# Optimization experiments

Hardware: AMD Instinct MI355X
Metric: run time of the kernel (lower is better)

The kernel has to match this reference:

```python
import jax, jax.numpy as jnp
import numpy as np

B = 8
H1c = W1c = 56
H2c = W2c = 112
C1 = 512
C2 = 256
NH = 8
WS = 7
POOL = 2
EPS = 1e-5


def setup_inputs() -> dict:
    key = jax.random.key(0)
    ks = jax.random.split(key, 8)
    x = jax.random.normal(ks[0], (B, H1c * W1c, C1), dtype=jnp.float32)
    y = jax.random.normal(ks[1], (B, H2c * W2c, C2), dtype=jnp.float32)
    Wq = jax.random.normal(ks[2], (C1, C1), dtype=jnp.float32) * 0.02
    Wkv = jax.random.normal(ks[3], (2 * C1, C2), dtype=jnp.float32) * 0.02
    Wproj = jax.random.normal(ks[4], (C1, C1), dtype=jnp.float32) * 0.02
    bproj = jnp.zeros((C1,), dtype=jnp.float32)
    # 1x1 conv: fan_out = out_channels -> std = sqrt(2/C2)
    Wsr = jax.random.normal(ks[5], (C2, C2), dtype=jnp.float32) * np.sqrt(2.0 / C2).astype(np.float32)
    bsr = jnp.zeros((C2,), dtype=jnp.float32)
    gn = jnp.ones((C2,), dtype=jnp.float32)
    bn = jnp.zeros((C2,), dtype=jnp.float32)
    return {"x": x, "y": y, "Wq": Wq, "Wkv": Wkv, "Wproj": Wproj,
            "bproj": bproj, "Wsr": Wsr, "bsr": bsr, "gn": gn, "bn": bn,
            "H1": H1c, "W1": W1c, "H2": H2c, "W2": W2c}


def _window_partition(t, ws):
    # t: (B, nh, H, W, C) -> (B*nh, num_windows, ws*ws, C)
    Bt, n, H, W, C = t.shape
    ht, wt = H // ws, W // ws
    t = t.reshape(Bt, n, ht, ws, wt, ws, C).transpose(0, 1, 2, 4, 3, 5, 6)
    return t.reshape(Bt * n, ht * wt, ws * ws, C)


def reference(x, y, Wq, Wkv, Wproj, bproj, Wsr, bsr, gn, bn, H1, W1, H2, W2):
    B1, N1, c1 = x.shape
    B2, N2, c2 = y.shape
    nh, ws = NH, WS
    hd = c1 // nh
    scale = hd ** (-0.5)

    # q projection -> (B, nh, H1, W1, hd)
    q = (x @ Wq.T).reshape(B1, H1, W1, nh, hd).transpose(0, 3, 1, 2, 4)

    # KV preprocessing: avgpool -> 1x1 conv -> layernorm -> gelu
    y2 = y.transpose(0, 2, 1).reshape(B2, c2, H2, W2)
    Hp, Wp = H2 // POOL, W2 // POOL
    y2 = y2.reshape(B2, c2, Hp, POOL, Wp, POOL).mean(axis=(3, 5))
    y2 = jnp.einsum('bchw,oc->bohw', y2, Wsr) + bsr[None, :, None, None]
    y2 = y2.reshape(B2, c2, Hp * Wp).transpose(0, 2, 1)  # (B, Np, C2)
    mu = y2.mean(-1, keepdims=True)
    var = y2.var(-1, keepdims=True)
    y2 = (y2 - mu) / jnp.sqrt(var + EPS) * gn + bn
    y2 = jax.nn.gelu(y2, approximate=False)

    kv = (y2 @ Wkv.T).reshape(B2, Hp * Wp, 2, nh, hd)
    k = kv[:, :, 0].transpose(0, 2, 1, 3).reshape(B2, nh, Hp, Wp, hd)
    v = kv[:, :, 1].transpose(0, 2, 1, 3).reshape(B2, nh, Hp, Wp, hd)

    qw = _window_partition(q, ws)   # (B*nh, nw, ws^2, hd)
    kw = _window_partition(k, ws)
    vw = _window_partition(v, ws)

    attn = jax.nn.softmax(jnp.einsum('bnqd,bnkd->bnqk', qw, kw) * scale, axis=-1)
    out = jnp.einsum('bnqk,bnkd->bnqd', attn, vw)  # (B*nh, nw, ws^2, hd)

    # window reverse -> (B, N1, C1)
    ht, wt = H1 // ws, W1 // ws
    out = out.reshape(B1, nh, ht, wt, ws, ws, hd).transpose(0, 1, 2, 4, 3, 5, 6)
    out = out.reshape(B1, nh, H1 * W1, hd).transpose(0, 2, 1, 3).reshape(B1, H1 * W1, c1)
    return out @ Wproj.T + bproj
```

## Files before the change

### kernel.cpp

```cpp
#include <hip/hip_runtime.h>
#include <hip/hip_bf16.h>

typedef __attribute__((ext_vector_type(8))) short short8;
typedef __attribute__((ext_vector_type(4))) float f32x4;
typedef __attribute__((ext_vector_type(4))) unsigned short ushort4v;

#define DI __device__ __forceinline__

DI unsigned short f2bf(float f) {
  union { float f; unsigned int u; } a; a.f = f;
  unsigned int u = a.u;
  return (unsigned short)((u + 0x7FFFu + ((u >> 16) & 1u)) >> 16);
}

#define BARRIER() do { asm volatile("" ::: "memory"); __builtin_amdgcn_s_barrier(); asm volatile("" ::: "memory"); } while (0)
#define GLOAD16(src, dst) __builtin_amdgcn_global_load_lds( \
    (const __attribute__((address_space(1))) void*)(src), \
    (__attribute__((address_space(3))) void*)(dst), 16, 0, 0)


__global__ __launch_bounds__(256)
void cvt_pool(const float* __restrict__ y, unsigned short* __restrict__ pooled,
              const float* __restrict__ Wq, const float* __restrict__ Wkv,
              const float* __restrict__ Wproj, const float* __restrict__ Wsr,
              unsigned short* __restrict__ Wq_b, unsigned short* __restrict__ Wkv_b,
              unsigned short* __restrict__ Wproj_b, unsigned short* __restrict__ Wsr_b) {
  int bid = blockIdx.x;
  if (bid < 6272) {
    int t = bid * 256 + threadIdx.x;
    int cv = (t & 63) * 4;
    int bp = t >> 6;
    int b = bp / 3136, p = bp % 3136;
    int hp = p / 56, wp = p % 56;
    const float* src = y + (((size_t)b * 12544) + hp * 224 + wp * 2) * 256 + cv;
    float4 a0 = *(const float4*)(src);
    float4 a1 = *(const float4*)(src + 256);
    float4 a2 = *(const float4*)(src + 28672);
    float4 a3 = *(const float4*)(src + 28672 + 256);
    float4 av;
    av.x = (a0.x + a1.x + a2.x + a3.x) * 0.25f;
    av.y = (a0.y + a1.y + a2.y + a3.y) * 0.25f;
    av.z = (a0.z + a1.z + a2.z + a3.z) * 0.25f;
    av.w = (a0.w + a1.w + a2.w + a3.w) * 0.25f;
    ushort4v o = { f2bf(av.x), f2bf(av.y), f2bf(av.z), f2bf(av.w) };
    *(ushort4v*)&pooled[(size_t)bp * 256 + cv] = o;
  } else {
    long i = (long)(bid - 6272) * 1024 + threadIdx.x * 4;
    const float* src; unsigned short* dst; long off;
    if (i < 262144L)      { src = Wq;    dst = Wq_b;    off = i; }
    else if (i < 524288L) { src = Wkv;   dst = Wkv_b;   off = i - 262144L; }
    else if (i < 786432L) { src = Wproj; dst = Wproj_b; off = i - 524288L; }
    else                  { src = Wsr;   dst = Wsr_b;   off = i - 786432L; }
    float4 v = *(const float4*)&src[off];
    ushort4v o = { f2bf(v.x), f2bf(v.y), f2bf(v.z), f2bf(v.w) };
    *(ushort4v*)&dst[off] = o;
  }
}

__global__ __launch_bounds__(256)
void sr_gemm(const unsigned short* __restrict__ Ap, const unsigned short* __restrict__ Wsr_b,
             const float* __restrict__ bsr, const float* __restrict__ gn,
             const float* __restrict__ bn, unsigned short* __restrict__ out) {
  __shared__ unsigned short sA[64 * 64];
  __shared__ unsigned short sB[256 * 64];
  __shared__ float red[64 * 8];

  const int tid = threadIdx.x;
  const int wv = tid >> 6;
  const int lane = tid & 63;
  const int lr = lane & 15;
  const int lg = lane >> 4;
  const int lr4 = lg * 4;
  const int m0 = blockIdx.x * 64;
  const int sr8 = lane >> 3;
  const int sl8 = lane & 7;

  f32x4 acc[4][4];
#pragma unroll
  for (int i = 0; i < 4; ++i)
#pragma unroll
    for (int j = 0; j < 4; ++j) acc[i][j] = (f32x4){0.f, 0.f, 0.f, 0.f};

  for (int kt = 0; kt < 256; kt += 64) {
#pragma unroll
    for (int c = 0; c < 2; ++c) {
      int row = wv * 16 + c * 8 + sr8;
      GLOAD16(Ap + (size_t)(m0 + row) * 256 + kt + ((sl8 ^ (row & 7)) * 8),
              &sA[(wv * 16 + c * 8) * 64]);
    }
#pragma unroll
    for (int c = 0; c < 8; ++c) {
      int row = wv * 64 + c * 8 + sr8;
      GLOAD16(Wsr_b + (size_t)row * 256 + kt + ((sl8 ^ (row & 7)) * 8),
              &sB[(wv * 64 + c * 8) * 64]);
    }
    __syncthreads();
#pragma unroll
    for (int ks = 0; ks < 2; ++ks) {
      short8 af[4], bfr[4];
#pragma unroll
      for (int i = 0; i < 4; ++i)
        af[i] = *(const short8*)&sA[(i * 16 + lr) * 64 + (((ks * 4 + lg) ^ (lr & 7)) * 8)];
#pragma unroll
      for (int j = 0; j < 4; ++j)
        bfr[j] = *(const short8*)&sB[(wv * 64 + j * 16 + lr) * 64 + (((ks * 4 + lg) ^ (lr & 7)) * 8)];
#pragma unroll
      for (int i = 0; i < 4; ++i)
#pragma unroll
        for (int j = 0; j < 4; ++j)
          acc[i][j] = __builtin_amdgcn_mfma_f32_16x16x32_bf16(af[i], bfr[j], acc[i][j], 0, 0, 0);
    }
    __syncthreads();
  }

  float bsv[4], gnv[4], bnv[4];
#pragma unroll
  for (int j = 0; j < 4; ++j) {
    int col = wv * 64 + j * 16 + lr;
    bsv[j] = bsr[col]; gnv[j] = gn[col]; bnv[j] = bn[col];
  }
  float s_[4][4], q_[4][4];
#pragma unroll
  for (int i = 0; i < 4; ++i)
#pragma unroll
    for (int r = 0; r < 4; ++r) {
      float s = 0.f, q = 0.f;
#pragma unroll
      for (int j = 0; j < 4; ++j) {
        float v = acc[i][j][r] + bsv[j];
        acc[i][j][r] = v;
        s += v; q += v * v;
      }
      s_[i][r] = s; q_[i][r] = q;
    }
#pragma unroll
  for (int m = 1; m <= 8; m <<= 1)
#pragma unroll
    for (int i = 0; i < 4; ++i)
#pragma unroll
      for (int r = 0; r < 4; ++r) {
        s_[i][r] += __shfl_xor(s_[i][r], m);
        q_[i][r] += __shfl_xor(q_[i][r], m);
      }
  if (lr == 0) {
#pragma unroll
    for (int i = 0; i < 4; ++i)
#pragma unroll
      for (int r = 0; r < 4; ++r) {
        int row = i * 16 + lr4 + r;
        red[row * 8 + wv * 2 + 0] = s_[i][r];
        red[row * 8 + wv * 2 + 1] = q_[i][r];
      }
  }
  __syncthreads();
#pragma unroll
  for (int i = 0; i < 4; ++i) {
#pragma unroll
    for (int r = 0; r < 4; ++r) {
      int row = i * 16 + lr4 + r;
      float sum = red[row * 8 + 0] + red[row * 8 + 2] + red[row * 8 + 4] + red[row * 8 + 6];
      float sq  = red[row * 8 + 1] + red[row * 8 + 3] + red[row * 8 + 5] + red[row * 8 + 7];
      float mean = sum * (1.f / 256.f);
      float var = sq * (1.f / 256.f) - mean * mean;
      float rstd = rsqrtf(var + 1e-5f);
#pragma unroll
      for (int j = 0; j < 4; ++j) {
        float t = (acc[i][j][r] - mean) * rstd * gnv[j] + bnv[j];
        t = 0.5f * t * (1.f + erff(t * 0.70710678118654752f));
        out[(size_t)(m0 + row) * 256 + wv * 64 + j * 16 + lr] = f2bf(t);
      }
    }
  }
}

DI void epi_q(int gm, int gc, float v, unsigned short* outp) {
  const int b = gm / 3136, pos = gm % 3136;
  const int h = pos / 56, ww = pos % 56;
  const int head = gc >> 6, d = gc & 63;
  const size_t idx = ((((size_t)(b * 8 + head)) * 64 + (h / 7) * 8 + (ww / 7)) * 49
                      + (h % 7) * 7 + (ww % 7)) * 64 + d;
  outp[idx] = f2bf(v);
}

template<int K, int N>
__global__ __launch_bounds__(512, 2)
void gemm256f(const float* __restrict__ A,
              const unsigned short* __restrict__ Bw,
              unsigned short* __restrict__ outp) {
  __shared__ unsigned short lds[65536];
  const int tid = threadIdx.x;
  const int wv = tid >> 6;
  const int lane = tid & 63;
  const int wm = wv >> 2;
  const int wn = wv & 3;
  const int m0 = blockIdx.y * 256;
  const int n0 = blockIdx.x * 256;
  const int lr = lane & 15;
  const int lg = lane >> 4;
  const int lr4 = lg * 4;
  const int srow8 = lane >> 3;
  const int sl8 = lane & 7;
  constexpr int NT = K / 64;

  f32x4 acc[8][4];
#pragma unroll
  for (int i = 0; i < 8; ++i)
#pragma unroll
    for (int j = 0; j < 4; ++j) acc[i][j] = (f32x4){0.f, 0.f, 0.f, 0.f};

  float4 fa[4][2];
  auto loadA = [&](int t1) {
    int tsrc = (t1 < NT) ? t1 : NT - 1;
#pragma unroll
    for (int rr = 0; rr < 4; ++rr) {
      int trow = rr * 64 + wv * 8 + srow8;
      const float* p = A + (size_t)(m0 + trow) * K + tsrc * 64 + sl8 * 8;
      fa[rr][0] = *(const float4*)p;
      fa[rr][1] = *(const float4*)(p + 4);
    }
    asm volatile("" ::: "memory");
  };
  auto writeA = [&](int t1) {
#pragma unroll
    for (int rr = 0; rr < 4; ++rr) {
      int trow = rr * 64 + wv * 8 + srow8;
      union { short8 s; unsigned short u[8]; } w;
      w.u[0] = f2bf(fa[rr][0].x); w.u[1] = f2bf(fa[rr][0].y);
      w.u[2] = f2bf(fa[rr][0].z); w.u[3] = f2bf(fa[rr][0].w);
      w.u[4] = f2bf(fa[rr][1].x); w.u[5] = f2bf(fa[rr][1].y);
      w.u[6] = f2bf(fa[rr][1].z); w.u[7] = f2bf(fa[rr][1].w);
      *(short8*)&lds[(t1 & 1) * 32768 + trow * 64 + ((sl8 ^ (trow & 7)) * 8)] = w.s;
    }
  };
  auto stageB = [&](int t1, int rr) {
    int tsrc = (t1 < NT) ? t1 : NT - 1;
    int trow = rr * 64 + wv * 8 + srow8;
    int sx = sl8 ^ (trow & 7);
    GLOAD16(Bw + (size_t)(n0 + trow) * K + tsrc * 64 + sx * 8,
            &lds[(t1 & 1) * 32768 + 16384 + (rr * 64 + wv * 8) * 64]);
  };
  auto rdA = [&](int s, int mf, int ks) -> short8 {
    int row = wm * 128 + mf * 16 + lr;
    int slot = ((ks << 2) + lg) ^ (row & 7);
    return *(const short8*)&lds[s * 32768 + row * 64 + slot * 8];
  };
  auto rdB = [&](int s, int nf, int ks) -> short8 {
    int row = wn * 64 + nf * 16 + lr;
    int slot = ((ks << 2) + lg) ^ (row & 7);
    return *(const short8*)&lds[s * 32768 + 16384 + row * 64 + slot * 8];
  };

  stageB(0, 0); stageB(0, 1); stageB(0, 2); stageB(0, 3);
  loadA(0);
  asm volatile("s_waitcnt vmcnt(0)" ::: "memory");
  writeA(0);
  asm volatile("s_waitcnt lgkmcnt(0)" ::: "memory");
  BARRIER();

  for (int t = 0; t < NT; ++t) {
    const int s = t & 1;
    short8 bfr[4][2];
    loadA(t + 1);
#pragma unroll
    for (int j = 0; j < 4; ++j) { bfr[j][0] = rdB(s, j, 0); bfr[j][1] = rdB(s, j, 1); }
    {
      short8 x0 = rdA(s, 0, 0), x1 = rdA(s, 0, 1);
      short8 y0 = rdA(s, 1, 0), y1 = rdA(s, 1, 1);
      BARRIER();
      __builtin_amdgcn_s_setprio(1);
#pragma unroll
      for (int j = 0; j < 4; ++j) {
        acc[0][j] = __builtin_amdgcn_mfma_f32_16x16x32_bf16(x0, bfr[j][0], acc[0][j], 0, 0, 0);
        acc[0][j] = __builtin_amdgcn_mfma_f32_16x16x32_bf16(x1, bfr[j][1], acc[0][j], 0, 0, 0);
        acc[1][j] = __builtin_amdgcn_mfma_f32_16x16x32_bf16(y0, bfr[j][0], acc[1][j], 0, 0, 0);
        acc[1][j] = __builtin_amdgcn_mfma_f32_16x16x32_bf16(y1, bfr[j][1], acc[1][j], 0, 0, 0);
      }
      __builtin_amdgcn_s_setprio(0);
      BARRIER();
    }
    stageB(t + 1, 0); stageB(t + 1, 1);
    {
      short8 x0 = rdA(s, 2, 0), x1 = rdA(s, 2, 1);
      short8 y0 = rdA(s, 3, 0), y1 = rdA(s, 3, 1);
      BARRIER();
      __builtin_amdgcn_s_setprio(1);
#pragma unroll
      for (int j = 0; j < 4; ++j) {
        acc[2][j] = __builtin_amdgcn_mfma_f32_16x16x32_bf16(x0, bfr[j][0], acc[2][j], 0, 0, 0);
        acc[2][j] = __builtin_amdgcn_mfma_f32_16x16x32_bf16(x1, bfr[j][1], acc[2][j], 0, 0, 0);
        acc[3][j] = __builtin_amdgcn_mfma_f32_16x16x32_bf16(y0, bfr[j][0], acc[3][j], 0, 0, 0);
        acc[3][j] = __builtin_amdgcn_mfma_f32_16x16x32_bf16(y1, bfr[j][1], acc[3][j], 0, 0, 0);
      }
      __builtin_amdgcn_s_setprio(0);
      BARRIER();
    }
    stageB(t + 1, 2); stageB(t + 1, 3);
    {
      short8 x0 = rdA(s, 4, 0), x1 = rdA(s, 4, 1);
      short8 y0 = rdA(s, 5, 0), y1 = rdA(s, 5, 1);
      BARRIER();
      __builtin_amdgcn_s_setprio(1);
#pragma unroll
      for (int j = 0; j < 4; ++j) {
        acc[4][j] = __builtin_amdgcn_mfma_f32_16x16x32_bf16(x0, bfr[j][0], acc[4][j], 0, 0, 0);
        acc[4][j] = __builtin_amdgcn_mfma_f32_16x16x32_bf16(x1, bfr[j][1], acc[4][j], 0, 0, 0);
        acc[5][j] = __builtin_amdgcn_mfma_f32_16x16x32_bf16(y0, bfr[j][0], acc[5][j], 0, 0, 0);
        acc[5][j] = __builtin_amdgcn_mfma_f32_16x16x32_bf16(y1, bfr[j][1], acc[5][j], 0, 0, 0);
      }
      __builtin_amdgcn_s_setprio(0);
      BARRIER();
    }
    {
      short8 x0 = rdA(s, 6, 0), x1 = rdA(s, 6, 1);
      short8 y0 = rdA(s, 7, 0), y1 = rdA(s, 7, 1);
      asm volatile("s_waitcnt vmcnt(4)" ::: "memory");
      writeA(t + 1);
      asm volatile("s_waitcnt lgkmcnt(0)" ::: "memory");
      BARRIER();
      __builtin_amdgcn_s_setprio(1);
#pragma unroll
      for (int j = 0; j < 4; ++j) {
        acc[6][j] = __builtin_amdgcn_mfma_f32_16x16x32_bf16(x0, bfr[j][0], acc[6][j], 0, 0, 0);
        acc[6][j] = __builtin_amdgcn_mfma_f32_16x16x32_bf16(x1, bfr[j][1], acc[6][j], 0, 0, 0);
        acc[7][j] = __builtin_amdgcn_mfma_f32_16x16x32_bf16(y0, bfr[j][0], acc[7][j], 0, 0, 0);
        acc[7][j] = __builtin_amdgcn_mfma_f32_16x16x32_bf16(y1, bfr[j][1], acc[7][j], 0, 0, 0);
      }
      __builtin_amdgcn_s_setprio(0);
      asm volatile("s_waitcnt vmcnt(0)" ::: "memory");
      BARRIER();
    }
  }

#pragma unroll
  for (int i = 0; i < 8; ++i)
#pragma unroll
    for (int j = 0; j < 4; ++j)
#pragma unroll
      for (int r = 0; r < 4; ++r)
        epi_q(m0 + wm * 128 + i * 16 + lr4 + r, n0 + wn * 64 + j * 16 + lr,
              acc[i][j][r], outp);
}

__global__ __launch_bounds__(512)
void kvattn(const unsigned short* __restrict__ y2,
            const unsigned short* __restrict__ Wkv_b,
            const unsigned short* __restrict__ qwin,
            const unsigned short* __restrict__ Wproj_b,
            const float* __restrict__ bproj,
            float* __restrict__ out) {
  __shared__ unsigned short lds[81920];
  const int tid = threadIdx.x;
  const int wv = tid >> 6;
  const int lane = tid & 63;
  const int lr = lane & 15;
  const int lg = lane >> 4;
  const int r8 = lane >> 3;
  const int sl8 = lane & 7;
  const int bb = blockIdx.x >> 6;
  const int win = blockIdx.x & 63;
  const int ht = win >> 3, wt = win & 7;

  unsigned short* Cy = lds;
  unsigned short* SL = lds + 16384 + wv * 8192;
  unsigned short* OA = lds + 16384;
  unsigned short* WP = lds + 49152 + wv * 4096;

  {
    int m = wv * 8 + r8;
    int mm = (m < 49) ? m : 48;
    int grow = bb * 3136 + (ht * 7 + mm / 7) * 56 + wt * 7 + (mm % 7);
#pragma unroll
    for (int kt = 0; kt < 4; ++kt)
      GLOAD16(y2 + (size_t)grow * 256 + kt * 64 + ((sl8 ^ (m & 7)) * 8),
              &Cy[kt * 4096 + wv * 8 * 64]);
  }

  auto stageW = [&](int s) {
    int h2 = s >> 2, kt = s & 3;
#pragma unroll
    for (int c = 0; c < 8; ++c) {
      int lrow = c * 8 + r8;
      GLOAD16(Wkv_b + (size_t)(h2 * 512 + wv * 64 + lrow) * 256 + kt * 64 + ((sl8 ^ (lrow & 7)) * 8),
              &SL[(s & 1) * 4096 + c * 8 * 64]);
    }
  };

  f32x4 aK[4][4], aV[4][4];
#pragma unroll
  for (int i = 0; i < 4; ++i)
#pragma unroll
    for (int j = 0; j < 4; ++j) { aK[i][j] = (f32x4){0,0,0,0}; aV[i][j] = (f32x4){0,0,0,0}; }

  stageW(0);
  asm volatile("s_waitcnt vmcnt(8)" ::: "memory");
  BARRIER();

#pragma unroll
  for (int s = 0; s < 8; ++s) {
    if (s < 7) {
      stageW(s + 1);
      asm volatile("s_waitcnt vmcnt(8)" ::: "memory");
    } else {
      asm volatile("s_waitcnt vmcnt(0)" ::: "memory");
    }
    const int kt = s & 3;
    const unsigned short* Wb = &SL[(s & 1) * 4096];
    short8 bfrg[4][2];
#pragma unroll
    for (int nf = 0; nf < 4; ++nf)
#pragma unroll
      for (int ks = 0; ks < 2; ++ks)
        bfrg[nf][ks] = *(const short8*)&Wb[(nf * 16 + lr) * 64 + (((ks * 4 + lg) ^ (lr & 7)) * 8)];
#pragma unroll
    for (int mf = 0; mf < 4; ++mf)
#pragma unroll
      for (int ks = 0; ks < 2; ++ks) {
        short8 af = *(const short8*)&Cy[kt * 4096 + (mf * 16 + lr) * 64 + (((ks * 4 + lg) ^ (lr & 7)) * 8)];
#pragma unroll
        for (int nf = 0; nf < 4; ++nf) {
          if (s < 4)
            aK[mf][nf] = __builtin_amdgcn_mfma_f32_16x16x32_bf16(af, bfrg[nf][ks], aK[mf][nf], 0, 0, 0);
          else
            aV[mf][nf] = __builtin_amdgcn_mfma_f32_16x16x32_bf16(af, bfrg[nf][ks], aV[mf][nf], 0, 0, 0);
        }
      }
  }

  const unsigned short* qb = qwin + (size_t)((bb * 8 + wv) * 64 + win) * 3136;
  short8 qf[4][2];
#pragma unroll
  for (int mf = 0; mf < 4; ++mf)
#pragma unroll
    for (int ks = 0; ks < 2; ++ks)
      qf[mf][ks] = *(const short8*)&qb[(mf * 16 + lr) * 64 + ks * 32 + lg * 8];

#pragma unroll
  for (int mf = 0; mf < 4; ++mf)
#pragma unroll
    for (int nf = 0; nf < 4; ++nf)
#pragma unroll
      for (int r = 0; r < 4; ++r) {
        int key = mf * 16 + lg * 4 + r;
        int d = nf * 16 + lr;
        SL[key * 64 + (((d >> 3) ^ (key & 7)) * 8) + (d & 7)] = f2bf(aK[mf][nf][r]);
        SL[4096 + d * 64 + (((key >> 3) ^ (d & 7)) * 8) + (key & 7)] = f2bf(aV[mf][nf][r]);
      }

  f32x4 aS[4][4];
#pragma unroll
  for (int i = 0; i < 4; ++i)
#pragma unroll
    for (int j = 0; j < 4; ++j) aS[i][j] = (f32x4){0,0,0,0};
#pragma unroll
  for (int mf = 0; mf < 4; ++mf)
#pragma unroll
    for (int ks = 0; ks < 2; ++ks)
#pragma unroll
      for (int nf = 0; nf < 4; ++nf) {
        short8 bk = *(const short8*)&SL[(nf * 16 + lr) * 64 + (((ks * 4 + lg) ^ (lr & 7)) * 8)];
        aS[mf][nf] = __builtin_amdgcn_mfma_f32_16x16x32_bf16(qf[mf][ks], bk, aS[mf][nf], 0, 0, 0);
      }

#pragma unroll
  for (int nf = 0; nf < 4; ++nf)
    if (nf * 16 + lr >= 49) {
#pragma unroll
      for (int mf = 0; mf < 4; ++mf)
#pragma unroll
        for (int r = 0; r < 4; ++r) aS[mf][nf][r] = -1e30f;
    }
  const float cexp = 0.125f * 1.4426950408889634f;
  float mx[4][4], sm[4][4];
#pragma unroll
  for (int mf = 0; mf < 4; ++mf)
#pragma unroll
    for (int r = 0; r < 4; ++r)
      mx[mf][r] = fmaxf(fmaxf(aS[mf][0][r], aS[mf][1][r]), fmaxf(aS[mf][2][r], aS[mf][3][r]));
#pragma unroll
  for (int m = 1; m <= 8; m <<= 1)
#pragma unroll
    for (int mf = 0; mf < 4; ++mf)
#pragma unroll
      for (int r = 0; r < 4; ++r) mx[mf][r] = fmaxf(mx[mf][r], __shfl_xor(mx[mf][r], m));
#pragma unroll
  for (int mf = 0; mf < 4; ++mf)
#pragma unroll
    for (int nf = 0; nf < 4; ++nf)
#pragma unroll
      for (int r = 0; r < 4; ++r)
        aS[mf][nf][r] = exp2f((aS[mf][nf][r] - mx[mf][r]) * cexp);
#pragma unroll
  for (int mf = 0; mf < 4; ++mf)
#pragma unroll
    for (int r = 0; r < 4; ++r)
      sm[mf][r] = aS[mf][0][r] + aS[mf][1][r] + aS[mf][2][r] + aS[mf][3][r];
#pragma unroll
  for (int m = 1; m <= 8; m <<= 1)
#pragma unroll
    for (int mf = 0; mf < 4; ++mf)
#pragma unroll
      for (int r = 0; r < 4; ++r) sm[mf][r] += __shfl_xor(sm[mf][r], m);
#pragma unroll
  for (int mf = 0; mf < 4; ++mf)
#pragma unroll
    for (int r = 0; r < 4; ++r) sm[mf][r] = 1.f / sm[mf][r];

#pragma unroll
  for (int mf = 0; mf < 4; ++mf)
#pragma unroll
    for (int nf = 0; nf < 4; ++nf)
#pragma unroll
      for (int r = 0; r < 4; ++r) {
        int q = mf * 16 + lg * 4 + r;
        int key = nf * 16 + lr;
        SL[q * 64 + (((key >> 3) ^ (q & 7)) * 8) + (key & 7)] = f2bf(aS[mf][nf][r] * sm[mf][r]);
      }

  f32x4 aO[4][4];
#pragma unroll
  for (int i = 0; i < 4; ++i)
#pragma unroll
    for (int j = 0; j < 4; ++j) aO[i][j] = (f32x4){0,0,0,0};
#pragma unroll
  for (int mf = 0; mf < 4; ++mf)
#pragma unroll
    for (int ks = 0; ks < 2; ++ks) {
      short8 pf = *(const short8*)&SL[(mf * 16 + lr) * 64 + (((ks * 4 + lg) ^ (lr & 7)) * 8)];
#pragma unroll
      for (int df = 0; df < 4; ++df) {
        short8 vf = *(const short8*)&SL[4096 + (df * 16 + lr) * 64 + (((ks * 4 + lg) ^ (lr & 7)) * 8)];
        aO[mf][df] = __builtin_amdgcn_mfma_f32_16x16x32_bf16(pf, vf, aO[mf][df], 0, 0, 0);
      }
    }

  BARRIER();
#pragma unroll
  for (int mf = 0; mf < 4; ++mf)
#pragma unroll
    for (int nf = 0; nf < 4; ++nf)
#pragma unroll
      for (int r = 0; r < 4; ++r) {
        int q = mf * 16 + lg * 4 + r;
        int slot = nf * 2 + (lr >> 3);
        OA[q * 512 + wv * 64 + ((slot ^ (q & 7)) * 8) + (lr & 7)] = f2bf(aO[mf][nf][r]);
      }
  {
    short8 nx[8];
#pragma unroll
    for (int c = 0; c < 8; ++c) {
      int lrow = c * 8 + r8;
      nx[c] = *(const short8*)&Wproj_b[(size_t)(wv * 64 + lrow) * 512 + ((sl8 ^ (lrow & 7)) * 8)];
    }
#pragma unroll
    for (int c = 0; c < 8; ++c)
      *(short8*)&WP[(c * 8 + r8) * 64 + sl8 * 8] = nx[c];
  }
  BARRIER();

  f32x4 aR[4][4];
#pragma unroll
  for (int i = 0; i < 4; ++i)
#pragma unroll
    for (int j = 0; j < 4; ++j) aR[i][j] = (f32x4){0,0,0,0};
#pragma unroll
  for (int kt = 0; kt < 8; ++kt) {
    short8 nx[8];
    if (kt < 7) {
#pragma unroll
      for (int c = 0; c < 8; ++c) {
        int lrow = c * 8 + r8;
        nx[c] = *(const short8*)&Wproj_b[(size_t)(wv * 64 + lrow) * 512 + (kt + 1) * 64 + ((sl8 ^ (lrow & 7)) * 8)];
      }
    }
#pragma unroll
    for (int mf = 0; mf < 4; ++mf)
#pragma unroll
      for (int ks = 0; ks < 2; ++ks) {
        short8 af = *(const short8*)&OA[(mf * 16 + lr) * 512 + kt * 64 + (((ks * 4 + lg) ^ (lr & 7)) * 8)];
#pragma unroll
        for (int nf = 0; nf < 4; ++nf) {
          short8 bf2 = *(const short8*)&WP[(nf * 16 + lr) * 64 + (((ks * 4 + lg) ^ (lr & 7)) * 8)];
          aR[mf][nf] = __builtin_amdgcn_mfma_f32_16x16x32_bf16(af, bf2, aR[mf][nf], 0, 0, 0);
        }
      }
    if (kt < 7) {
#pragma unroll
      for (int c = 0; c < 8; ++c)
        *(short8*)&WP[(c * 8 + r8) * 64 + sl8 * 8] = nx[c];
    }
  }

#pragma unroll
  for (int mf = 0; mf < 4; ++mf)
#pragma unroll
    for (int nf = 0; nf < 4; ++nf)
#pragma unroll
      for (int r = 0; r < 4; ++r) {
        int q = mf * 16 + lg * 4 + r;
        if (q < 49) {
          int gm = bb * 3136 + (ht * 7 + q / 7) * 56 + wt * 7 + (q % 7);
          int col = wv * 64 + nf * 16 + lr;
          out[(size_t)gm * 512 + col] = aR[mf][nf][r] + bproj[col];
        }
      }
}

extern "C" void kernel_launch(void* const* d_in, const int* in_sizes, int n_in,
                              void* d_out, int out_size, void* d_ws, size_t ws_size,
                              hipStream_t stream) {
  const float* x     = (const float*)d_in[0];
  const float* y     = (const float*)d_in[1];
  const float* Wq    = (const float*)d_in[2];
  const float* Wkv   = (const float*)d_in[3];
  const float* Wproj = (const float*)d_in[4];
  const float* bproj = (const float*)d_in[5];
  const float* Wsr   = (const float*)d_in[6];
  const float* bsr   = (const float*)d_in[7];
  const float* gn    = (const float*)d_in[8];
  const float* bn    = (const float*)d_in[9];
  float* out = (float*)d_out;

  char* ws = (char*)d_ws;
  unsigned short* Wq_b    = (unsigned short*)ws; ws += 524288;
  unsigned short* Wkv_b   = (unsigned short*)ws; ws += 524288;
  unsigned short* Wproj_b = (unsigned short*)ws; ws += 524288;
  unsigned short* Wsr_b   = (unsigned short*)ws; ws += 131072;
  unsigned short* regA    = (unsigned short*)ws; ws += 12845056;
  unsigned short* q_win   = (unsigned short*)ws; ws += 25690112;
  unsigned short* regC    = (unsigned short*)ws; ws += 12845056;

  cvt_pool<<<7104, 256, 0, stream>>>(y, regA, Wq, Wkv, Wproj, Wsr,
                                     Wq_b, Wkv_b, Wproj_b, Wsr_b);

  gemm256f<512, 512><<<dim3(2, 98), 512, 0, stream>>>(x, Wq_b, q_win);

  sr_gemm<<<392, 256, 0, stream>>>(regA, Wsr_b, bsr, gn, bn, regC);

  kvattn<<<512, 512, 0, stream>>>(regC, Wkv_b, q_win, Wproj_b, bproj, out);
}
```

Measured before the change: 141.4 us.

## Split each head across two waves in kvattn with 1024-thread blocks

Doubles the kvattn block to 16 waves so that each attention head is handled by a pair of waves. Each wave computes half of the K/V columns, half of the query rows and half of the projection output columns. This cuts per-wave register use and serial MFMA chains, aiming for more latency hiding with the same grid. In exchange it adds block-wide barriers between stages and shares LDS buffers per head. The Wproj prologue now uses async global-to-LDS loads.

```diff
diff --git a/kernel.cpp b/kernel.cpp
--- a/kernel.cpp
+++ b/kernel.cpp
@@ -341,7 +341,7 @@
               acc[i][j][r], outp);
 }
 
-__global__ __launch_bounds__(512)
+__global__ __launch_bounds__(1024)
 void kvattn(const unsigned short* __restrict__ y2,
             const unsigned short* __restrict__ Wkv_b,
             const unsigned short* __restrict__ qwin,
@@ -350,7 +350,9 @@
             float* __restrict__ out) {
   __shared__ unsigned short lds[81920];
   const int tid = threadIdx.x;
-  const int wv = tid >> 6;
+  const int wv16 = tid >> 6;
+  const int head = wv16 >> 1;
+  const int half = wv16 & 1;
   const int lane = tid & 63;
   const int lr = lane & 15;
   const int lg = lane >> 4;
@@ -360,216 +362,227 @@
   const int win = blockIdx.x & 63;
   const int ht = win >> 3, wt = win & 7;
 
-  unsigned short* Cy = lds;
-  unsigned short* SL = lds + 16384 + wv * 8192;
-  unsigned short* OA = lds + 16384;
-  unsigned short* WP = lds + 49152 + wv * 4096;
+  unsigned short* Cy  = lds;
+  unsigned short* SLh = lds + 16384 + head * 8192;
+  unsigned short* OA  = lds + 16384;
+  unsigned short* WPs = lds + 49152 + wv16 * 2048;
 
   {
-    int m = wv * 8 + r8;
+    int rb = wv16 & 7;
+    int m = rb * 8 + r8;
     int mm = (m < 49) ? m : 48;
     int grow = bb * 3136 + (ht * 7 + mm / 7) * 56 + wt * 7 + (mm % 7);
-#pragma unroll
-    for (int kt = 0; kt < 4; ++kt)
-      GLOAD16(y2 + (size_t)grow * 256 + kt * 64 + ((sl8 ^ (m & 7)) * 8),
-              &Cy[kt * 4096 + wv * 8 * 64]);
+    int p0 = wv16 >> 3;
+#pragma unroll
+    for (int pp = 0; pp < 2; ++pp) {
+      int panel = p0 + pp * 2;
+      GLOAD16(y2 + (size_t)grow * 256 + panel * 64 + ((sl8 ^ (m & 7)) * 8),
+              &Cy[panel * 4096 + rb * 512]);
+    }
   }
 
   auto stageW = [&](int s) {
     int h2 = s >> 2, kt = s & 3;
 #pragma unroll
-    for (int c = 0; c < 8; ++c) {
-      int lrow = c * 8 + r8;
-      GLOAD16(Wkv_b + (size_t)(h2 * 512 + wv * 64 + lrow) * 256 + kt * 64 + ((sl8 ^ (lrow & 7)) * 8),
-              &SL[(s & 1) * 4096 + c * 8 * 64]);
+    for (int c = 0; c < 4; ++c) {
+      int lrow = half * 32 + c * 8 + r8;
+      GLOAD16(Wkv_b + (size_t)(h2 * 512 + head * 64 + lrow) * 256 + kt * 64 + ((sl8 ^ r8) * 8),
+              &SLh[(s & 1) * 4096 + (half * 32 + c * 8) * 64]);
     }
   };
 
-  f32x4 aK[4][4], aV[4][4];
+  f32x4 aK[4][2], aV[4][2];
 #pragma unroll
   for (int i = 0; i < 4; ++i)
 #pragma unroll
-    for (int j = 0; j < 4; ++j) { aK[i][j] = (f32x4){0,0,0,0}; aV[i][j] = (f32x4){0,0,0,0}; }
+    for (int j = 0; j < 2; ++j) { aK[i][j] = (f32x4){0,0,0,0}; aV[i][j] = (f32x4){0,0,0,0}; }
 
   stageW(0);
-  asm volatile("s_waitcnt vmcnt(8)" ::: "memory");
+  asm volatile("s_waitcnt vmcnt(4)" ::: "memory");
   BARRIER();
 
 #pragma unroll
   for (int s = 0; s < 8; ++s) {
     if (s < 7) {
       stageW(s + 1);
-      asm volatile("s_waitcnt vmcnt(8)" ::: "memory");
+      asm volatile("s_waitcnt vmcnt(4)" ::: "memory");
     } else {
       asm volatile("s_waitcnt vmcnt(0)" ::: "memory");
     }
     const int kt = s & 3;
-    const unsigned short* Wb = &SL[(s & 1) * 4096];
-    short8 bfrg[4][2];
-#pragma unroll
-    for (int nf = 0; nf < 4; ++nf)
-#pragma unroll
-      for (int ks = 0; ks < 2; ++ks)
-        bfrg[nf][ks] = *(const short8*)&Wb[(nf * 16 + lr) * 64 + (((ks * 4 + lg) ^ (lr & 7)) * 8)];
+    const unsigned short* Wb = &SLh[(s & 1) * 4096];
+    short8 bfrg[2][2];
+#pragma unroll
+    for (int nf2 = 0; nf2 < 2; ++nf2)
+#pragma unroll
+      for (int ks = 0; ks < 2; ++ks) {
+        int row = (half * 2 + nf2) * 16 + lr;
+        bfrg[nf2][ks] = *(const short8*)&Wb[row * 64 + (((ks * 4 + lg) ^ (lr & 7)) * 8)];
+      }
 #pragma unroll
     for (int mf = 0; mf < 4; ++mf)
 #pragma unroll
       for (int ks = 0; ks < 2; ++ks) {
         short8 af = *(const short8*)&Cy[kt * 4096 + (mf * 16 + lr) * 64 + (((ks * 4 + lg) ^ (lr & 7)) * 8)];
 #pragma unroll
-        for (int nf = 0; nf < 4; ++nf) {
+        for (int nf2 = 0; nf2 < 2; ++nf2) {
           if (s < 4)
-            aK[mf][nf] = __builtin_amdgcn_mfma_f32_16x16x32_bf16(af, bfrg[nf][ks], aK[mf][nf], 0, 0, 0);
+            aK[mf][nf2] = __builtin_amdgcn_mfma_f32_16x16x32_bf16(af, bfrg[nf2][ks], aK[mf][nf2], 0, 0, 0);
           else
-            aV[mf][nf] = __builtin_amdgcn_mfma_f32_16x16x32_bf16(af, bfrg[nf][ks], aV[mf][nf], 0, 0, 0);
+            aV[mf][nf2] = __builtin_amdgcn_mfma_f32_16x16x32_bf16(af, bfrg[nf2][ks], aV[mf][nf2], 0, 0, 0);
         }
       }
   }
 
-  const unsigned short* qb = qwin + (size_t)((bb * 8 + wv) * 64 + win) * 3136;
-  short8 qf[4][2];
+  const unsigned short* qb = qwin + (size_t)((bb * 8 + head) * 64 + win) * 3136;
+  short8 qf[2][2];
+#pragma unroll
+  for (int mf2 = 0; mf2 < 2; ++mf2)
+#pragma unroll
+    for (int ks = 0; ks < 2; ++ks)
+      qf[mf2][ks] = *(const short8*)&qb[((half * 2 + mf2) * 16 + lr) * 64 + ks * 32 + lg * 8];
+
+  BARRIER();
+
 #pragma unroll
   for (int mf = 0; mf < 4; ++mf)
 #pragma unroll
-    for (int ks = 0; ks < 2; ++ks)
-      qf[mf][ks] = *(const short8*)&qb[(mf * 16 + lr) * 64 + ks * 32 + lg * 8];
-
-#pragma unroll
-  for (int mf = 0; mf < 4; ++mf)
-#pragma unroll
-    for (int nf = 0; nf < 4; ++nf)
+    for (int nf2 = 0; nf2 < 2; ++nf2)
 #pragma unroll
       for (int r = 0; r < 4; ++r) {
         int key = mf * 16 + lg * 4 + r;
-        int d = nf * 16 + lr;
-        SL[key * 64 + (((d >> 3) ^ (key & 7)) * 8) + (d & 7)] = f2bf(aK[mf][nf][r]);
-        SL[4096 + d * 64 + (((key >> 3) ^ (d & 7)) * 8) + (key & 7)] = f2bf(aV[mf][nf][r]);
-      }
-
-  f32x4 aS[4][4];
-#pragma unroll
-  for (int i = 0; i < 4; ++i)
+        int d = (half * 2 + nf2) * 16 + lr;
+        SLh[key * 64 + (((d >> 3) ^ (key & 7)) * 8) + (d & 7)] = f2bf(aK[mf][nf2][r]);
+        SLh[4096 + d * 64 + (((key >> 3) ^ (d & 7)) * 8) + (key & 7)] = f2bf(aV[mf][nf2][r]);
+      }
+  asm volatile("s_waitcnt lgkmcnt(0)" ::: "memory");
+  BARRIER();
+
+  f32x4 aS[2][4];
+#pragma unroll
+  for (int i = 0; i < 2; ++i)
 #pragma unroll
     for (int j = 0; j < 4; ++j) aS[i][j] = (f32x4){0,0,0,0};
 #pragma unroll
-  for (int mf = 0; mf < 4; ++mf)
+  for (int mf2 = 0; mf2 < 2; ++mf2)
 #pragma unroll
     for (int ks = 0; ks < 2; ++ks)
 #pragma unroll
       for (int nf = 0; nf < 4; ++nf) {
-        short8 bk = *(const short8*)&SL[(nf * 16 + lr) * 64 + (((ks * 4 + lg) ^ (lr & 7)) * 8)];
-        aS[mf][nf] = __builtin_amdgcn_mfma_f32_16x16x32_bf16(qf[mf][ks], bk, aS[mf][nf], 0, 0, 0);
+        short8 bk = *(const short8*)&SLh[(nf * 16 + lr) * 64 + (((ks * 4 + lg) ^ (lr & 7)) * 8)];
+        aS[mf2][nf] = __builtin_amdgcn_mfma_f32_16x16x32_bf16(qf[mf2][ks], bk, aS[mf2][nf], 0, 0, 0);
       }
 
 #pragma unroll
   for (int nf = 0; nf < 4; ++nf)
     if (nf * 16 + lr >= 49) {
 #pragma unroll
-      for (int mf = 0; mf < 4; ++mf)
-#pragma unroll
-        for (int r = 0; r < 4; ++r) aS[mf][nf][r] = -1e30f;
+      for (int mf2 = 0; mf2 < 2; ++mf2)
+#pragma unroll
+        for (int r = 0; r < 4; ++r) aS[mf2][nf][r] = -1e30f;
     }
   const float cexp = 0.125f * 1.4426950408889634f;
-  float mx[4][4], sm[4][4];
-#pragma unroll
-  for (int mf = 0; mf < 4; ++mf)
+  float mx[2][4], sm[2][4];
+#pragma unroll
+  for (int mf2 = 0; mf2 < 2; ++mf2)
 #pragma unroll
     for (int r = 0; r < 4; ++r)
-      mx[mf][r] = fmaxf(fmaxf(aS[mf][0][r], aS[mf][1][r]), fmaxf(aS[mf][2][r], aS[mf][3][r]));
+      mx[mf2][r] = fmaxf(fmaxf(aS[mf2][0][r], aS[mf2][1][r]), fmaxf(aS[mf2][2][r], aS[mf2][3][r]));
 #pragma unroll
   for (int m = 1; m <= 8; m <<= 1)
 #pragma unroll
-    for (int mf = 0; mf < 4; ++mf)
-#pragma unroll
-      for (int r = 0; r < 4; ++r) mx[mf][r] = fmaxf(mx[mf][r], __shfl_xor(mx[mf][r], m));
-#pragma unroll
-  for (int mf = 0; mf < 4; ++mf)
+    for (int mf2 = 0; mf2 < 2; ++mf2)
+#pragma unroll
+      for (int r = 0; r < 4; ++r) mx[mf2][r] = fmaxf(mx[mf2][r], __shfl_xor(mx[mf2][r], m));
+#pragma unroll
+  for (int mf2 = 0; mf2 < 2; ++mf2)
 #pragma unroll
     for (int nf = 0; nf < 4; ++nf)
 #pragma unroll
       for (int r = 0; r < 4; ++r)
-        aS[mf][nf][r] = exp2f((aS[mf][nf][r] - mx[mf][r]) * cexp);
-#pragma unroll
-  for (int mf = 0; mf < 4; ++mf)
+        aS[mf2][nf][r] = exp2f((aS[mf2][nf][r] - mx[mf2][r]) * cexp);
+#pragma unroll
+  for (int mf2 = 0; mf2 < 2; ++mf2)
 #pragma unroll
     for (int r = 0; r < 4; ++r)
-      sm[mf][r] = aS[mf][0][r] + aS[mf][1][r] + aS[mf][2][r] + aS[mf][3][r];
+      sm[mf2][r] = aS[mf2][0][r] + aS[mf2][1][r] + aS[mf2][2][r] + aS[mf2][3][r];
 #pragma unroll
   for (int m = 1; m <= 8; m <<= 1)
 #pragma unroll
-    for (int mf = 0; mf < 4; ++mf)
-#pragma unroll
-      for (int r = 0; r < 4; ++r) sm[mf][r] += __shfl_xor(sm[mf][r], m);
-#pragma unroll
-  for (int mf = 0; mf < 4; ++mf)
-#pragma unroll
-    for (int r = 0; r < 4; ++r) sm[mf][r] = 1.f / sm[mf][r];
-
-#pragma unroll
-  for (int mf = 0; mf < 4; ++mf)
+    for (int mf2 = 0; mf2 < 2; ++mf2)
+#pragma unroll
+      for (int r = 0; r < 4; ++r) sm[mf2][r] += __shfl_xor(sm[mf2][r], m);
+#pragma unroll
+  for (int mf2 = 0; mf2 < 2; ++mf2)
+#pragma unroll
+    for (int r = 0; r < 4; ++r) sm[mf2][r] = 1.f / sm[mf2][r];
+
+  BARRIER();
+
+#pragma unroll
+  for (int mf2 = 0; mf2 < 2; ++mf2)
 #pragma unroll
     for (int nf = 0; nf < 4; ++nf)
 #pragma unroll
       for (int r = 0; r < 4; ++r) {
-        int q = mf * 16 + lg * 4 + r;
+        int q = (half * 2 + mf2) * 16 + lg * 4 + r;
         int key = nf * 16 + lr;
-        SL[q * 64 + (((key >> 3) ^ (q & 7)) * 8) + (key & 7)] = f2bf(aS[mf][nf][r] * sm[mf][r]);
-      }
-
-  f32x4 aO[4][4];
+        SLh[q * 64 + (((key >> 3) ^ (q & 7)) * 8) + (key & 7)] = f2bf(aS[mf2][nf][r] * sm[mf2][r]);
+      }
+
+  f32x4 aO[2][4];
+#pragma unroll
+  for (int i = 0; i < 2; ++i)
+#pragma unroll
+    for (int j = 0; j < 4; ++j) aO[i][j] = (f32x4){0,0,0,0};
+#pragma unroll
+  for (int mf2 = 0; mf2 < 2; ++mf2)
+#pragma unroll
+    for (int ks = 0; ks < 2; ++ks) {
+      int qrow = (half * 2 + mf2) * 16 + lr;
+      short8 pf = *(const short8*)&SLh[qrow * 64 + (((ks * 4 + lg) ^ (lr & 7)) * 8)];
+#pragma unroll
+      for (int df = 0; df < 4; ++df) {
+        short8 vf = *(const short8*)&SLh[4096 + (df * 16 + lr) * 64 + (((ks * 4 + lg) ^ (lr & 7)) * 8)];
+        aO[mf2][df] = __builtin_amdgcn_mfma_f32_16x16x32_bf16(pf, vf, aO[mf2][df], 0, 0, 0);
+      }
+    }
+
+  BARRIER();
+
+#pragma unroll
+  for (int mf2 = 0; mf2 < 2; ++mf2)
+#pragma unroll
+    for (int df = 0; df < 4; ++df)
+#pragma unroll
+      for (int r = 0; r < 4; ++r) {
+        int q = (half * 2 + mf2) * 16 + lg * 4 + r;
+        int slot = df * 2 + (lr >> 3);
+        OA[q * 512 + head * 64 + ((slot ^ (q & 7)) * 8) + (lr & 7)] = f2bf(aO[mf2][df][r]);
+      }
+#pragma unroll
+  for (int c = 0; c < 4; ++c) {
+    int lrow = c * 8 + r8;
+    GLOAD16(Wproj_b + (size_t)(head * 64 + half * 32 + lrow) * 512 + ((sl8 ^ r8) * 8),
+            &WPs[c * 512]);
+  }
+  asm volatile("s_waitcnt lgkmcnt(0) vmcnt(0)" ::: "memory");
+  BARRIER();
+
+  f32x4 aR[4][2];
 #pragma unroll
   for (int i = 0; i < 4; ++i)
 #pragma unroll
-    for (int j = 0; j < 4; ++j) aO[i][j] = (f32x4){0,0,0,0};
-#pragma unroll
-  for (int mf = 0; mf < 4; ++mf)
-#pragma unroll
-    for (int ks = 0; ks < 2; ++ks) {
-      short8 pf = *(const short8*)&SL[(mf * 16 + lr) * 64 + (((ks * 4 + lg) ^ (lr & 7)) * 8)];
-#pragma unroll
-      for (int df = 0; df < 4; ++df) {
-        short8 vf = *(const short8*)&SL[4096 + (df * 16 + lr) * 64 + (((ks * 4 + lg) ^ (lr & 7)) * 8)];
-        aO[mf][df] = __builtin_amdgcn_mfma_f32_16x16x32_bf16(pf, vf, aO[mf][df], 0, 0, 0);
-      }
-    }
-
-  BARRIER();
-#pragma unroll
-  for (int mf = 0; mf < 4; ++mf)
-#pragma unroll
-    for (int nf = 0; nf < 4; ++nf)
-#pragma unroll
-      for (int r = 0; r < 4; ++r) {
-        int q = mf * 16 + lg * 4 + r;
-        int slot = nf * 2 + (lr >> 3);
-        OA[q * 512 + wv * 64 + ((slot ^ (q & 7)) * 8) + (lr & 7)] = f2bf(aO[mf][nf][r]);
-      }
-  {
-    short8 nx[8];
-#pragma unroll
-    for (int c = 0; c < 8; ++c) {
-      int lrow = c * 8 + r8;
-      nx[c] = *(const short8*)&Wproj_b[(size_t)(wv * 64 + lrow) * 512 + ((sl8 ^ (lrow & 7)) * 8)];
-    }
-#pragma unroll
-    for (int c = 0; c < 8; ++c)
-      *(short8*)&WP[(c * 8 + r8) * 64 + sl8 * 8] = nx[c];
-  }
-  BARRIER();
-
-  f32x4 aR[4][4];
-#pragma unroll
-  for (int i = 0; i < 4; ++i)
-#pragma unroll
-    for (int j = 0; j < 4; ++j) aR[i][j] = (f32x4){0,0,0,0};
+    for (int j = 0; j < 2; ++j) aR[i][j] = (f32x4){0,0,0,0};
 #pragma unroll
   for (int kt = 0; kt < 8; ++kt) {
-    short8 nx[8];
+    short8 nx[4];
     if (kt < 7) {
 #pragma unroll
-      for (int c = 0; c < 8; ++c) {
+      for (int c = 0; c < 4; ++c) {
         int lrow = c * 8 + r8;
-        nx[c] = *(const short8*)&Wproj_b[(size_t)(wv * 64 + lrow) * 512 + (kt + 1) * 64 + ((sl8 ^ (lrow & 7)) * 8)];
+        nx[c] = *(const short8*)&Wproj_b[(size_t)(head * 64 + half * 32 + lrow) * 512
+                                         + (kt + 1) * 64 + ((sl8 ^ r8) * 8)];
       }
     }
 #pragma unroll
@@ -578,29 +591,29 @@
       for (int ks = 0; ks < 2; ++ks) {
         short8 af = *(const short8*)&OA[(mf * 16 + lr) * 512 + kt * 64 + (((ks * 4 + lg) ^ (lr & 7)) * 8)];
 #pragma unroll
-        for (int nf = 0; nf < 4; ++nf) {
-          short8 bf2 = *(const short8*)&WP[(nf * 16 + lr) * 64 + (((ks * 4 + lg) ^ (lr & 7)) * 8)];
-          aR[mf][nf] = __builtin_amdgcn_mfma_f32_16x16x32_bf16(af, bf2, aR[mf][nf], 0, 0, 0);
+        for (int nf2 = 0; nf2 < 2; ++nf2) {
+          short8 bf2 = *(const short8*)&WPs[(nf2 * 16 + lr) * 64 + (((ks * 4 + lg) ^ (lr & 7)) * 8)];
+          aR[mf][nf2] = __builtin_amdgcn_mfma_f32_16x16x32_bf16(af, bf2, aR[mf][nf2], 0, 0, 0);
         }
       }
     if (kt < 7) {
 #pragma unroll
-      for (int c = 0; c < 8; ++c)
-        *(short8*)&WP[(c * 8 + r8) * 64 + sl8 * 8] = nx[c];
+      for (int c = 0; c < 4; ++c)
+        *(short8*)&WPs[(c * 8 + r8) * 64 + sl8 * 8] = nx[c];
     }
   }
 
 #pragma unroll
   for (int mf = 0; mf < 4; ++mf)
 #pragma unroll
-    for (int nf = 0; nf < 4; ++nf)
+    for (int nf2 = 0; nf2 < 2; ++nf2)
 #pragma unroll
       for (int r = 0; r < 4; ++r) {
         int q = mf * 16 + lg * 4 + r;
         if (q < 49) {
           int gm = bb * 3136 + (ht * 7 + q / 7) * 56 + wt * 7 + (q % 7);
-          int col = wv * 64 + nf * 16 + lr;
-          out[(size_t)gm * 512 + col] = aR[mf][nf][r] + bproj[col];
+          int col = head * 64 + (half * 2 + nf2) * 16 + lr;
+          out[(size_t)gm * 512 + col] = aR[mf][nf2][r] + bproj[col];
         }
       }
 }
@@ -636,5 +649,5 @@
 
   sr_gemm<<<392, 256, 0, stream>>>(regA, Wsr_b, bsr, gn, bn, regC);
 
-  kvattn<<<512, 512, 0, stream>>>(regC, Wkv_b, q_win, Wproj_b, bproj, out);
+  kvattn<<<512, 1024, 0, stream>>>(regC, Wkv_b, q_win, Wproj_b, bproj, out);
 }
```

Result: no change. 139.8 us (-1.1%).
